# Optimization experiments

Measured on AMD Instinct MI355X. Metric: run time of the kernel, lower is better.

## Reference

```python
import jax, jax.numpy as jnp
import numpy as np

D_MODEL = 2048
NUM_HEADS = 16
D_HEAD = D_MODEL // NUM_HEADS
MAX_SEQ_LEN = 2048
THETA = 10000.0


def setup_inputs() -> dict:
    key = jax.random.key(0)
    kx, kq, kk, kv, ko = jax.random.split(key, 5)
    std = float(np.sqrt(2.0 / (D_MODEL + D_MODEL)))
    def tn(k):
        # truncated normal in [-3std, 3std] scaled by std
        return std * jax.random.truncated_normal(k, -3.0, 3.0, (D_MODEL, D_MODEL), jnp.float32)
    return {
        "x": jax.random.normal(kx, (2, MAX_SEQ_LEN, D_MODEL), jnp.float32),
        "w_q": tn(kq),
        "w_k": tn(kk),
        "w_v": tn(kv),
        "w_o": tn(ko),
    }


def _rope(x):
    # x: [B, H, S, Dh], default positions = arange(S)
    S = x.shape[-2]
    pos = jnp.arange(S, dtype=jnp.float32)
    inv_freq = 1.0 / (THETA ** (jnp.arange(0, D_HEAD, 2, dtype=jnp.float32) / D_HEAD))
    ang = pos[:, None] * inv_freq[None, :]           # [S, Dh/2]
    cos = jnp.cos(ang).astype(x.dtype)
    sin = jnp.sin(ang).astype(x.dtype)
    x_even = x[..., 0::2]
    x_odd = x[..., 1::2]
    out_even = x_even * cos - x_odd * sin
    out_odd = x_even * sin + x_odd * cos
    # interleave even/odd back
    return jnp.stack([out_even, out_odd], axis=-1).reshape(x.shape)


def reference(x, w_q, w_k, w_v, w_o):
    B, S, _ = x.shape
    def split_heads(t):
        return t.reshape(B, S, NUM_HEADS, D_HEAD).transpose(0, 2, 1, 3)  # [B,H,S,Dh]
    q = split_heads(x @ w_q.T)
    k = split_heads(x @ w_k.T)
    v = split_heads(x @ w_v.T)
    q = _rope(q)
    k = _rope(k)
    scores = jnp.einsum('bhqd,bhkd->bhqk', q, k) / jnp.sqrt(jnp.asarray(D_HEAD, x.dtype))
    causal = jnp.tril(jnp.ones((S, S), dtype=bool))
    scores = jnp.where(causal, scores, jnp.finfo(scores.dtype).min)
    attn = jax.nn.softmax(scores, axis=-1)
    out = jnp.einsum('bhqk,bhkd->bhqd', attn, v)     # [B,H,S,Dh]
    out = out.transpose(0, 2, 1, 3).reshape(B, S, D_MODEL)
    return out @ w_o.T
```

## Files before the change

kernel.cpp:

```cpp
#include <hip/hip_runtime.h>
#include <hip/hip_bf16.h>

typedef __bf16 bf16;
typedef __bf16 bf16x8 __attribute__((ext_vector_type(8)));
typedef __bf16 bf16x4 __attribute__((ext_vector_type(4)));
typedef float f32x4 __attribute__((ext_vector_type(4)));

#define MFMA_BF16(a, b, c) __builtin_amdgcn_mfma_f32_16x16x32_bf16(a, b, c, 0, 0, 0)

constexpr int D_MODEL = 2048;
constexpr int NUM_HEADS = 16;
constexpr int D_HEAD = 128;
constexpr int SEQ = 2048;
constexpr int BATCH = 2;
constexpr int M_TOTAL = BATCH * SEQ;

__device__ __forceinline__ void gld_lds16(const bf16* g, bf16* l) {
  __builtin_amdgcn_global_load_lds((const __attribute__((address_space(1))) void*)g,
                                   (__attribute__((address_space(3))) void*)l, 16, 0, 0);
}

__global__ __launch_bounds__(256) void cvt_f32_to_bf16(const float* __restrict__ src,
                                                       bf16* __restrict__ dst, int n4) {
  int i = blockIdx.x * 256 + threadIdx.x;
  if (i >= n4) return;
  float4 v = reinterpret_cast<const float4*>(src)[i];
  bf16x4 o;
  o[0] = (bf16)v.x; o[1] = (bf16)v.y; o[2] = (bf16)v.z; o[3] = (bf16)v.w;
  reinterpret_cast<bf16x4*>(dst)[i] = o;
}

enum { EP_F32 = 0, EP_QKV = 1 };

template <int EPI>
__global__ __launch_bounds__(256) void gemm_bt(const bf16* __restrict__ A,
                                               const bf16* __restrict__ B,
                                               void* __restrict__ C0,
                                               void* __restrict__ C1,
                                               void* __restrict__ C2,
                                               int M, int N, int K) {
  __shared__ __align__(16) bf16 As[128 * 32];
  __shared__ __align__(16) bf16 Bs[128 * 32];
  const int tid = threadIdx.x;
  const int lane = tid & 63;
  const int wave = tid >> 6;
  const int lane15 = lane & 15;
  const int quad = lane >> 4;
  const int m0 = blockIdx.y * 128;
  const int n0 = blockIdx.x * 128;
  const int wm = (wave >> 1) * 64;
  const int wn = (wave & 1) * 64;

  const int srow = wave * 16 + (lane >> 2);
  const int skc = ((lane & 3) ^ ((lane >> 3) & 3)) * 8;
  const bf16* gA = A + (long)(m0 + srow) * K + skc;
  const bf16* gB = B + (long)(n0 + srow) * K + skc;
  const long roff = (long)64 * K;
  bf16* lA0 = As + wave * 512;
  bf16* lA1 = As + 2048 + wave * 512;
  bf16* lB0 = Bs + wave * 512;
  bf16* lB1 = Bs + 2048 + wave * 512;
  const int swq = (quad ^ ((lane15 >> 1) & 3)) * 8;

  f32x4 acc[4][4];
#pragma unroll
  for (int i = 0; i < 4; ++i)
#pragma unroll
    for (int j = 0; j < 4; ++j) acc[i][j] = (f32x4){0.f, 0.f, 0.f, 0.f};

  for (int k0 = 0; k0 < K; k0 += 32) {
    __syncthreads();
    gld_lds16(gA + k0, lA0);
    gld_lds16(gA + roff + k0, lA1);
    gld_lds16(gB + k0, lB0);
    gld_lds16(gB + roff + k0, lB1);
    __syncthreads();

    bf16x8 af[4], bfr[4];
#pragma unroll
    for (int i = 0; i < 4; ++i)
      af[i] = *reinterpret_cast<const bf16x8*>(&As[(wm + i * 16 + lane15) * 32 + swq]);
#pragma unroll
    for (int j = 0; j < 4; ++j)
      bfr[j] = *reinterpret_cast<const bf16x8*>(&Bs[(wn + j * 16 + lane15) * 32 + swq]);
#pragma unroll
    for (int i = 0; i < 4; ++i)
#pragma unroll
      for (int j = 0; j < 4; ++j)
        acc[i][j] = MFMA_BF16(af[i], bfr[j], acc[i][j]);
  }

  if (EPI == EP_F32) {
#pragma unroll
    for (int i = 0; i < 4; ++i)
#pragma unroll
      for (int j = 0; j < 4; ++j)
#pragma unroll
        for (int r = 0; r < 4; ++r) {
          const int m = m0 + wm + i * 16 + quad * 4 + r;
          const int n = n0 + wn + j * 16 + lane15;
          reinterpret_cast<float*>(C0)[(long)m * N + n] = acc[i][j][r];
        }
  } else {
    const int mat = n0 >> 11;
    bf16* dst = (mat == 0) ? (bf16*)C0 : (mat == 1) ? (bf16*)C1 : (bf16*)C2;
    const int nb = n0 & 2047;
    if (mat < 2) {
#pragma unroll
      for (int i = 0; i < 4; ++i)
#pragma unroll
        for (int j = 0; j < 4; ++j)
#pragma unroll
          for (int r = 0; r < 4; ++r) {
            const int m = m0 + wm + i * 16 + quad * 4 + r;
            const int nl = nb + wn + j * 16 + lane15;
            const int b = m >> 11;
            const int s = m & (SEQ - 1);
            const int h = nl >> 7;
            const int d = nl & (D_HEAD - 1);
            float v = acc[i][j][r];
            float other = __shfl_xor(v, 1);
            float fr = exp2f((float)(d & ~1) * -0.103810253f);
            float ang = (float)s * fr;
            float sn = __sinf(ang);
            float cs = __cosf(ang);
            float outv = (lane15 & 1) ? (v * cs + other * sn) : (v * cs - other * sn);
            dst[(((long)(b * NUM_HEADS + h)) * SEQ + s) * D_HEAD + d] = (bf16)outv;
          }
    } else {
      const int h = nb >> 7;
#pragma unroll
      for (int i = 0; i < 4; ++i)
#pragma unroll
        for (int j = 0; j < 4; ++j) {
          bf16x4 pk;
#pragma unroll
          for (int r = 0; r < 4; ++r) pk[r] = (bf16)acc[i][j][r];
          const int m = m0 + wm + i * 16 + quad * 4;
          const int b = m >> 11;
          const int s = m & (SEQ - 1);
          const int d = wn + j * 16 + lane15;
          *reinterpret_cast<bf16x4*>(
              &dst[(((long)(b * NUM_HEADS + h)) * D_HEAD + d) * SEQ + s]) = pk;
        }
    }
  }
}

__global__ __launch_bounds__(256) void flash_attn(const bf16* __restrict__ Q,
                                                  const bf16* __restrict__ K,
                                                  const bf16* __restrict__ Vt,
                                                  bf16* __restrict__ O) {
  __shared__ __align__(16) bf16 Kl[64 * 128];
  __shared__ __align__(16) bf16 Vl[128 * 64];
  __shared__ __align__(16) bf16 P[4 * 16 * 72];
  const int tid = threadIdx.x;
  const int lane = tid & 63;
  const int wave = tid >> 6;
  const int lane15 = lane & 15;
  const int quad = lane >> 4;
  const int bh = blockIdx.x & 31;
  const int qcg = 31 - (blockIdx.x >> 5);
  const int q0 = qcg * 64 + wave * 16;
  const long base = (long)bh * SEQ * D_HEAD;
  const bf16* qp = Q + base;
  const bf16* kp = K + base;
  const bf16* vp = Vt + base;
  bf16* Pw = &P[wave * 16 * 72];
  constexpr float scale = 0.08838834764831845f;
  constexpr float SMAX = 30.0f;

  int ksrc[4], vsrc[4];
  const int kdst = wave * 512;
#pragma unroll
  for (int i = 0; i < 4; ++i) {
    const int c = i * 256 + tid;
    const int krow = c >> 4;
    ksrc[i] = krow * D_HEAD + (((c & 15) ^ (krow & 15)) * 8);
    const int vd = c >> 3;
    vsrc[i] = vd * SEQ + (((c & 7) ^ (vd & 7)) * 8);
  }

  bf16x8 bq[4];
#pragma unroll
  for (int kk = 0; kk < 4; ++kk)
    bq[kk] = *reinterpret_cast<const bf16x8*>(qp + (long)(q0 + lane15) * D_HEAD + kk * 32 + quad * 8);

  f32x4 o_acc[8];
#pragma unroll
  for (int dj = 0; dj < 8; ++dj) o_acc[dj] = (f32x4){0.f, 0.f, 0.f, 0.f};
  float l_part = 0.f;
  const int qcol = q0 + lane15;

  const int nkt = qcg + 1;
  for (int kt = 0; kt < nkt; ++kt) {
    const int k0 = kt * 64;

    __syncthreads();
#pragma unroll
    for (int i = 0; i < 4; ++i) gld_lds16(kp + k0 * D_HEAD + ksrc[i], Kl + i * 2048 + kdst);
#pragma unroll
    for (int i = 0; i < 4; ++i) gld_lds16(vp + k0 + vsrc[i], Vl + i * 2048 + kdst);
    __syncthreads();

    f32x4 sc[4];
#pragma unroll
    for (int j = 0; j < 4; ++j) sc[j] = (f32x4){0.f, 0.f, 0.f, 0.f};
#pragma unroll
    for (int j = 0; j < 4; ++j) {
#pragma unroll
      for (int kk = 0; kk < 4; ++kk) {
        bf16x8 ak = *reinterpret_cast<const bf16x8*>(
            &Kl[(j * 16 + lane15) * D_HEAD + (((kk * 4 + quad) ^ lane15) * 8)]);
        sc[j] = MFMA_BF16(ak, bq[kk], sc[j]);
      }
    }

#pragma unroll
    for (int j = 0; j < 4; ++j) {
      bf16x4 pk;
#pragma unroll
      for (int r = 0; r < 4; ++r) {
        const int kpos = k0 + j * 16 + quad * 4 + r;
        float p = (kpos <= qcol) ? __expf(sc[j][r] * scale - SMAX) : 0.f;
        l_part += p;
        pk[r] = (bf16)p;
      }
      *reinterpret_cast<bf16x4*>(&Pw[lane15 * 72 + j * 16 + quad * 4]) = pk;
    }

#pragma unroll
    for (int kc = 0; kc < 2; ++kc) {
      bf16x8 ap = *reinterpret_cast<const bf16x8*>(&Pw[lane15 * 72 + kc * 32 + quad * 8]);
#pragma unroll
      for (int dj = 0; dj < 8; ++dj) {
        bf16x8 bv = *reinterpret_cast<const bf16x8*>(
            &Vl[(dj * 16 + lane15) * 64 + (((kc * 4 + quad) ^ (lane15 & 7)) * 8)]);
        o_acc[dj] = MFMA_BF16(ap, bv, o_acc[dj]);
      }
    }
  }

  float lsum = l_part;
  lsum += __shfl_xor(lsum, 16);
  lsum += __shfl_xor(lsum, 32);

  const int b = bh >> 4;
  const int h = bh & 15;
#pragma unroll
  for (int r = 0; r < 4; ++r) {
    const float lr = __shfl(lsum, quad * 4 + r);
    const float inv_l = 1.0f / lr;
    const int qrow = q0 + quad * 4 + r;
#pragma unroll
    for (int dj = 0; dj < 8; ++dj)
      O[((long)b * SEQ + qrow) * D_MODEL + h * D_HEAD + dj * 16 + lane15] =
          (bf16)(o_acc[dj][r] * inv_l);
  }
}

extern "C" void kernel_launch(void* const* d_in, const int* in_sizes, int n_in,
                              void* d_out, int out_size, void* d_ws, size_t ws_size,
                              hipStream_t stream) {
  const float* x = (const float*)d_in[0];
  const float* wq = (const float*)d_in[1];
  const float* wk = (const float*)d_in[2];
  const float* wv = (const float*)d_in[3];
  const float* wo = (const float*)d_in[4];
  float* out = (float*)d_out;

  char* ws = (char*)d_ws;
  size_t off = 0;
  bf16* x_bf = (bf16*)(ws + off);  off += (size_t)M_TOTAL * D_MODEL * 2;
  bf16* wq_bf = (bf16*)(ws + off); off += (size_t)D_MODEL * D_MODEL * 2;
  bf16* wk_bf = (bf16*)(ws + off); off += (size_t)D_MODEL * D_MODEL * 2;
  bf16* wv_bf = (bf16*)(ws + off); off += (size_t)D_MODEL * D_MODEL * 2;
  bf16* wo_bf = (bf16*)(ws + off); off += (size_t)D_MODEL * D_MODEL * 2;
  bf16* q_r = (bf16*)(ws + off);   off += (size_t)M_TOTAL * D_MODEL * 2;
  bf16* k_r = (bf16*)(ws + off);   off += (size_t)M_TOTAL * D_MODEL * 2;
  bf16* vt_r = (bf16*)(ws + off);  off += (size_t)M_TOTAL * D_MODEL * 2;
  bf16* a_o = (bf16*)(ws + off);   off += (size_t)M_TOTAL * D_MODEL * 2;

  const int n4x = M_TOTAL * D_MODEL / 4;
  const int n4w = D_MODEL * D_MODEL / 4;
  cvt_f32_to_bf16<<<n4x / 256, 256, 0, stream>>>(x, x_bf, n4x);
  cvt_f32_to_bf16<<<n4w / 256, 256, 0, stream>>>(wq, wq_bf, n4w);
  cvt_f32_to_bf16<<<n4w / 256, 256, 0, stream>>>(wk, wk_bf, n4w);
  cvt_f32_to_bf16<<<n4w / 256, 256, 0, stream>>>(wv, wv_bf, n4w);
  cvt_f32_to_bf16<<<n4w / 256, 256, 0, stream>>>(wo, wo_bf, n4w);

  dim3 blk(256);
  gemm_bt<EP_QKV><<<dim3(3 * D_MODEL / 128, M_TOTAL / 128), blk, 0, stream>>>(
      x_bf, wq_bf, q_r, k_r, vt_r, M_TOTAL, 3 * D_MODEL, D_MODEL);

  flash_attn<<<dim3(1024), blk, 0, stream>>>(q_r, k_r, vt_r, a_o);

  gemm_bt<EP_F32><<<dim3(D_MODEL / 128, M_TOTAL / 128), blk, 0, stream>>>(
      a_o, wo_bf, out, nullptr, nullptr, M_TOTAL, D_MODEL, D_MODEL);
}
```

Baseline: 400.4 us.

## Double-buffer K/V tiles in flash attention and merge conversion kernels

```diff
diff --git a/kernel.cpp b/kernel.cpp
--- a/kernel.cpp
+++ b/kernel.cpp
@@ -20,11 +20,24 @@
                                    (__attribute__((address_space(3))) void*)l, 16, 0, 0);
 }
 
-__global__ __launch_bounds__(256) void cvt_f32_to_bf16(const float* __restrict__ src,
-                                                       bf16* __restrict__ dst, int n4) {
-  int i = blockIdx.x * 256 + threadIdx.x;
-  if (i >= n4) return;
-  float4 v = reinterpret_cast<const float4*>(src)[i];
+__global__ __launch_bounds__(256) void cvt_all(const float* __restrict__ x,
+                                               const float* __restrict__ wq,
+                                               const float* __restrict__ wk,
+                                               const float* __restrict__ wv,
+                                               const float* __restrict__ wo,
+                                               bf16* __restrict__ dst) {
+  const long i = (long)blockIdx.x * 256 + threadIdx.x;
+  const float* src;
+  long off;
+  if (i < 2097152) {
+    src = x; off = i;
+  } else {
+    const long j = i - 2097152;
+    const int w = (int)(j >> 20);
+    off = j & 1048575;
+    src = (w == 0) ? wq : (w == 1) ? wk : (w == 2) ? wv : wo;
+  }
+  float4 v = reinterpret_cast<const float4*>(src)[off];
   bf16x4 o;
   o[0] = (bf16)v.x; o[1] = (bf16)v.y; o[2] = (bf16)v.z; o[3] = (bf16)v.w;
   reinterpret_cast<bf16x4*>(dst)[i] = o;
@@ -151,16 +164,17 @@
                                                   const bf16* __restrict__ K,
                                                   const bf16* __restrict__ Vt,
                                                   bf16* __restrict__ O) {
-  __shared__ __align__(16) bf16 Kl[64 * 128];
-  __shared__ __align__(16) bf16 Vl[128 * 64];
+  __shared__ __align__(16) bf16 Kl[2][64 * 128];
+  __shared__ __align__(16) bf16 Vl[2][128 * 64];
   __shared__ __align__(16) bf16 P[4 * 16 * 72];
   const int tid = threadIdx.x;
   const int lane = tid & 63;
   const int wave = tid >> 6;
   const int lane15 = lane & 15;
   const int quad = lane >> 4;
-  const int bh = blockIdx.x & 31;
-  const int qcg = 31 - (blockIdx.x >> 5);
+  const int idx = blockIdx.x >> 3;
+  const int bh = (blockIdx.x & 7) * 4 + (idx & 3);
+  const int qcg = 31 - (idx >> 2);
   const int q0 = qcg * 64 + wave * 16;
   const long base = (long)bh * SEQ * D_HEAD;
   const bf16* qp = Q + base;
@@ -193,15 +207,24 @@
   const int qcol = q0 + lane15;
 
   const int nkt = qcg + 1;
+
+#pragma unroll
+  for (int i = 0; i < 4; ++i) gld_lds16(kp + ksrc[i], &Kl[0][i * 2048 + kdst]);
+#pragma unroll
+  for (int i = 0; i < 4; ++i) gld_lds16(vp + vsrc[i], &Vl[0][i * 2048 + kdst]);
+  __syncthreads();
+
   for (int kt = 0; kt < nkt; ++kt) {
     const int k0 = kt * 64;
-
-    __syncthreads();
-#pragma unroll
-    for (int i = 0; i < 4; ++i) gld_lds16(kp + k0 * D_HEAD + ksrc[i], Kl + i * 2048 + kdst);
-#pragma unroll
-    for (int i = 0; i < 4; ++i) gld_lds16(vp + k0 + vsrc[i], Vl + i * 2048 + kdst);
-    __syncthreads();
+    const int buf = kt & 1;
+
+    if (kt + 1 < nkt) {
+      const int nk0 = k0 + 64;
+#pragma unroll
+      for (int i = 0; i < 4; ++i) gld_lds16(kp + nk0 * D_HEAD + ksrc[i], &Kl[buf ^ 1][i * 2048 + kdst]);
+#pragma unroll
+      for (int i = 0; i < 4; ++i) gld_lds16(vp + nk0 + vsrc[i], &Vl[buf ^ 1][i * 2048 + kdst]);
+    }
 
     f32x4 sc[4];
 #pragma unroll
@@ -211,7 +234,7 @@
 #pragma unroll
       for (int kk = 0; kk < 4; ++kk) {
         bf16x8 ak = *reinterpret_cast<const bf16x8*>(
-            &Kl[(j * 16 + lane15) * D_HEAD + (((kk * 4 + quad) ^ lane15) * 8)]);
+            &Kl[buf][(j * 16 + lane15) * D_HEAD + (((kk * 4 + quad) ^ lane15) * 8)]);
         sc[j] = MFMA_BF16(ak, bq[kk], sc[j]);
       }
     }
@@ -235,10 +258,12 @@
 #pragma unroll
       for (int dj = 0; dj < 8; ++dj) {
         bf16x8 bv = *reinterpret_cast<const bf16x8*>(
-            &Vl[(dj * 16 + lane15) * 64 + (((kc * 4 + quad) ^ (lane15 & 7)) * 8)]);
+            &Vl[buf][(dj * 16 + lane15) * 64 + (((kc * 4 + quad) ^ (lane15 & 7)) * 8)]);
         o_acc[dj] = MFMA_BF16(ap, bv, o_acc[dj]);
       }
     }
+
+    __syncthreads();
   }
 
   float lsum = l_part;
@@ -281,15 +306,9 @@
   bf16* vt_r = (bf16*)(ws + off);  off += (size_t)M_TOTAL * D_MODEL * 2;
   bf16* a_o = (bf16*)(ws + off);   off += (size_t)M_TOTAL * D_MODEL * 2;
 
-  const int n4x = M_TOTAL * D_MODEL / 4;
-  const int n4w = D_MODEL * D_MODEL / 4;
-  cvt_f32_to_bf16<<<n4x / 256, 256, 0, stream>>>(x, x_bf, n4x);
-  cvt_f32_to_bf16<<<n4w / 256, 256, 0, stream>>>(wq, wq_bf, n4w);
-  cvt_f32_to_bf16<<<n4w / 256, 256, 0, stream>>>(wk, wk_bf, n4w);
-  cvt_f32_to_bf16<<<n4w / 256, 256, 0, stream>>>(wv, wv_bf, n4w);
-  cvt_f32_to_bf16<<<n4w / 256, 256, 0, stream>>>(wo, wo_bf, n4w);
-
   dim3 blk(256);
+  cvt_all<<<24576, blk, 0, stream>>>(x, wq, wk, wv, wo, x_bf);
+
   gemm_bt<EP_QKV><<<dim3(3 * D_MODEL / 128, M_TOTAL / 128), blk, 0, stream>>>(
       x_bf, wq_bf, q_r, k_r, vt_r, M_TOTAL, 3 * D_MODEL, D_MODEL);
 
```

New measurement: 390.9 us. -2.4%, faster.
